# Kernel tuning notes

Hardware: AMD Instinct MI355X
Metric: run time of the kernel (lower is better)

## Reference

```python
import jax, jax.numpy as jnp
import numpy as np

T, B, LAG, H = 128, 1024, 6, 256


def setup_inputs() -> dict:
    key = jax.random.key(0)
    ks = jax.random.split(key, 16)
    s = 0.05  # small init scale to keep LSTM gates in a sane range
    d = {}
    d["x"] = jax.random.normal(ks[0], (T, B, LAG), jnp.float32)
    d["Wi1"] = jax.random.normal(ks[1], (H, LAG), jnp.float32) * s
    d["bi1"] = jnp.zeros((H,), jnp.float32)
    d["Wi2"] = jax.random.normal(ks[2], (H, H), jnp.float32) * s
    d["bi2"] = jnp.zeros((H,), jnp.float32)
    d["Wi3"] = jax.random.normal(ks[3], (H, H), jnp.float32) * s
    d["bi3"] = jnp.zeros((H,), jnp.float32)
    d["Wih0"] = jax.random.normal(ks[4], (4 * H, H), jnp.float32) * s
    d["Whh0"] = jax.random.normal(ks[5], (4 * H, H), jnp.float32) * s
    d["bih0"] = jnp.zeros((4 * H,), jnp.float32)
    d["bhh0"] = jnp.zeros((4 * H,), jnp.float32)
    d["Wih1"] = jax.random.normal(ks[6], (4 * H, H), jnp.float32) * s
    d["Whh1"] = jax.random.normal(ks[7], (4 * H, H), jnp.float32) * s
    d["bih1"] = jnp.zeros((4 * H,), jnp.float32)
    d["bhh1"] = jnp.zeros((4 * H,), jnp.float32)
    d["Wo1"] = jax.random.normal(ks[8], (H, H), jnp.float32) * s
    d["bo1"] = jnp.zeros((H,), jnp.float32)
    d["Wo2"] = jax.random.normal(ks[9], (H, H), jnp.float32) * s
    d["bo2"] = jnp.zeros((H,), jnp.float32)
    d["Wo3"] = jax.random.normal(ks[10], (LAG, H), jnp.float32) * s
    d["bo3"] = jnp.zeros((LAG,), jnp.float32)
    return d


def _lstm_cell(xt, h, c, Wih, Whh, bih, bhh):
    # PyTorch gate order: i, f, g, o
    g = xt @ Wih.T + h @ Whh.T + (bih + bhh)
    i, f, gg, o = jnp.split(g, 4, axis=-1)
    c2 = jax.nn.sigmoid(f) * c + jax.nn.sigmoid(i) * jnp.tanh(gg)
    h2 = jax.nn.sigmoid(o) * jnp.tanh(c2)
    return h2, c2


def reference(x, Wi1, bi1, Wi2, bi2, Wi3, bi3,
              Wih0, Whh0, bih0, bhh0, Wih1, Whh1, bih1, bhh1,
              Wo1, bo1, Wo2, bo2, Wo3, bo3):
    relu = jax.nn.relu
    # input MLP applied to every timestep at once: [T,B,6] -> [T,B,H]
    u = relu(x @ Wi1.T + bi1)
    u = relu(u @ Wi2.T + bi2)
    u = relu(u @ Wi3.T + bi3)

    def step(carry, xt):
        h0, c0, h1, c1 = carry
        h0, c0 = _lstm_cell(xt, h0, c0, Wih0, Whh0, bih0, bhh0)
        # dropout(0.05) between layers is identity in eval mode
        h1, c1 = _lstm_cell(h0, h1, c1, Wih1, Whh1, bih1, bhh1)
        return (h0, c0, h1, c1), h1

    z = jnp.zeros((x.shape[1], Whh0.shape[1]), x.dtype)
    _, hs = jax.lax.scan(step, (z, z, z, z), u)  # hs: [T,B,H]

    # output MLP: ReLU, Linear, ReLU, Linear, ReLU, Linear(H->6)
    y = relu(hs)
    y = relu(y @ Wo1.T + bo1)
    y = relu(y @ Wo2.T + bo2)
    y = y @ Wo3.T + bo3
    return y  # [T,B,6]
```

## Files before the change

kernel.cpp:

```cpp
#include <hip/hip_runtime.h>
#include <math.h>


namespace {
constexpr int kT   = 128;
constexpr int kB   = 1024;
constexpr int kLag = 6;
constexpr int kH   = 256;
constexpr int kTc  = 32;
constexpr int kMc  = kTc * kB;
constexpr int kGS  = 67;
constexpr int kLdsBytes = 2 * 32768 + 2 * 64 * kGS * 4;
}

typedef _Float16 half8 __attribute__((ext_vector_type(8)));
typedef _Float16 half2 __attribute__((ext_vector_type(2)));
typedef float f32x4 __attribute__((ext_vector_type(4)));
typedef unsigned long long u64;

__device__ __forceinline__ float sigm(float x) {
    return 1.f / (1.f + exp2f(-1.4426950408889634f * x));
}
__device__ __forceinline__ float tanh_(float x) {
    return 2.f / (1.f + exp2f(-2.8853900817779268f * x)) - 1.f;
}

__device__ __forceinline__ half8 pack(u64 a, u64 b) {
    union { u64 u[2]; half8 h; } r;
    r.u[0] = a; r.u[1] = b;
    return r.h;
}

__device__ __forceinline__ void ld_l2(half8& d, const _Float16* p) {
    asm volatile("global_load_dwordx4 %0, %1, off sc0"
                 : "=v"(d) : "v"(p) : "memory");
}
#define WAITCNT_HOLD8(A, B)                                                   \
    asm volatile("s_waitcnt vmcnt(0)"                                         \
        : "+v"(A[0]), "+v"(A[1]), "+v"(A[2]), "+v"(A[3]),                     \
          "+v"(B[0]), "+v"(B[1]), "+v"(B[2]), "+v"(B[3]))

__global__ __launch_bounds__(256)
void zero_fill(unsigned int* __restrict__ p)
{
    p[blockIdx.x * 256 + threadIdx.x] = 0u;
}

__global__ __launch_bounds__(256)
void cvt_f2h(const float* __restrict__ s, _Float16* __restrict__ d)
{
    const int i = blockIdx.x * 256 + threadIdx.x;
    d[i] = (_Float16)s[i];
}

__global__ __launch_bounds__(256)
void build_wcat(const float* __restrict__ Wih, const float* __restrict__ Whh,
                _Float16* __restrict__ d)
{
    const int i = blockIdx.x * 256 + threadIdx.x;
    const int row = i >> 9, col = i & 511;
    const float v = (col < 256) ? Wih[row * 256 + col] : Whh[row * 256 + col - 256];
    d[i] = (_Float16)v;
}

__global__ __launch_bounds__(256)
void add_bias(const float* __restrict__ a, const float* __restrict__ b,
              float* __restrict__ d)
{
    const int i = blockIdx.x * 256 + threadIdx.x;
    d[i] = a[i] + b[i];
}

__global__ __launch_bounds__(256)
void in_mlp1(const float* __restrict__ x, const float* __restrict__ Wi1,
             const float* __restrict__ bi1, _Float16* __restrict__ out)
{
    const int idx = blockIdx.x * 256 + threadIdx.x;
    const int col = idx & (kH - 1);
    const int row = idx >> 8;
    const float* xr = x + (size_t)row * kLag;
    const float* w  = Wi1 + col * kLag;
    float s = bi1[col];
#pragma unroll
    for (int k = 0; k < kLag; ++k) s = fmaf(xr[k], w[k], s);
    out[idx] = (_Float16)fmaxf(s, 0.f);
}

__global__ __launch_bounds__(256)
void gemm_h16(const _Float16* __restrict__ A, const _Float16* __restrict__ W,
              const float* __restrict__ bias, _Float16* __restrict__ C)
{
    const int tid = threadIdx.x;
    const int w = tid >> 6, lane = tid & 63, q = lane >> 4, l15 = lane & 15;
    const int n0 = blockIdx.x * 64;
    const int r0 = blockIdx.y * 128 + w * 32;

    half8 bf[4][8];
#pragma unroll
    for (int nt = 0; nt < 4; ++nt)
#pragma unroll
        for (int kk = 0; kk < 8; ++kk)
            bf[nt][kk] = *(const half8*)(W + (size_t)(n0 + nt * 16 + l15) * 256
                                         + kk * 32 + q * 8);
    float bz[4];
#pragma unroll
    for (int nt = 0; nt < 4; ++nt) bz[nt] = bias[n0 + nt * 16 + l15];

#pragma unroll
    for (int rt = 0; rt < 2; ++rt) {
        const _Float16* arow = A + (size_t)(r0 + rt * 16 + l15) * 256 + q * 8;
        half8 af[8];
#pragma unroll
        for (int kk = 0; kk < 8; ++kk) af[kk] = *(const half8*)(arow + kk * 32);
        f32x4 acc[4];
#pragma unroll
        for (int nt = 0; nt < 4; ++nt)
            acc[nt] = (f32x4){bz[nt], bz[nt], bz[nt], bz[nt]};
#pragma unroll
        for (int kk = 0; kk < 8; ++kk)
#pragma unroll
            for (int nt = 0; nt < 4; ++nt)
                acc[nt] = __builtin_amdgcn_mfma_f32_16x16x32_f16(
                    af[kk], bf[nt][kk], acc[nt], 0, 0, 0);
#pragma unroll
        for (int nt = 0; nt < 4; ++nt)
#pragma unroll
            for (int r = 0; r < 4; ++r) {
                const float v = fmaxf(acc[nt][r], 0.f);
                C[(size_t)(r0 + rt * 16 + q * 4 + r) * 256 + n0 + nt * 16 + l15]
                    = (_Float16)v;
            }
    }
}

__device__ __forceinline__ void xbar(unsigned int* __restrict__ cptr,
                                     unsigned int target, int tid)
{
    asm volatile("s_waitcnt vmcnt(0)" ::: "memory");
    __syncthreads();
    if (tid == 0) {
        __hip_atomic_fetch_add(cptr, 1u, __ATOMIC_RELAXED,
                               __HIP_MEMORY_SCOPE_AGENT);
        while (__hip_atomic_load(cptr, __ATOMIC_RELAXED,
                                 __HIP_MEMORY_SCOPE_AGENT) < target)
            __builtin_amdgcn_s_sleep(1);
    }
    __syncthreads();
}

__device__ __forceinline__ void gather_lo(const _Float16* lo, int row, int q,
                                          u64* ua)
{
    const u64* plo = (const u64*)(lo + (size_t)row * 256 + q * 8);
#pragma unroll
    for (int kk = 0; kk < 8; ++kk) {
        ua[2*kk]   = plo[kk*8];
        ua[2*kk+1] = plo[kk*8 + 1];
    }
}

__device__ __forceinline__ void gstore(float* __restrict__ gl, int m0, int nb,
                                       int q, int l15,
                                       const f32x4& a0, const f32x4& a1)
{
#pragma unroll
    for (int r = 0; r < 4; ++r) {
        gl[(m0 + q*4 + r) * kGS + nb + l15]      = a0[r];
        gl[(m0 + q*4 + r) * kGS + nb + 16 + l15] = a1[r];
    }
}

__device__ __forceinline__ void phase_gemm_lds2(
    const char* pA, const char* pB,
    const half8 (&B0)[16], const half8 (&B1)[16],
    float* __restrict__ gl, int rtb, int nb, int q, int l15)
{
#pragma unroll
    for (int rt = 0; rt < 2; ++rt) {
        const int row = (rtb + rt) * 16 + l15;
        const int xr  = ((row & 15) << 4) ^ ((row & 1) << 8);
        const int rb  = row * 512;
        f32x4 a0 = {0.f,0.f,0.f,0.f}, a1 = {0.f,0.f,0.f,0.f};
#pragma unroll
        for (int kk = 0; kk < 8; ++kk) {
            const int off = rb + ((q * 16 + kk * 64) ^ xr);
            const half8 alo = *(const half8*)(pA + off);
            const half8 ahi = *(const half8*)(pB + off);
            a0 = __builtin_amdgcn_mfma_f32_16x16x32_f16(alo, B0[kk],     a0, 0,0,0);
            a1 = __builtin_amdgcn_mfma_f32_16x16x32_f16(alo, B1[kk],     a1, 0,0,0);
            a0 = __builtin_amdgcn_mfma_f32_16x16x32_f16(ahi, B0[8 + kk], a0, 0,0,0);
            a1 = __builtin_amdgcn_mfma_f32_16x16x32_f16(ahi, B1[8 + kk], a1, 0,0,0);
        }
        gstore(gl, (rtb + rt) * 16, nb, q, l15, a0, a1);
    }
}

__device__ __forceinline__ void phase_gemm_l0(
    const _Float16* __restrict__ u, const char* pH0,
    const half8 (&B0)[16], const half8 (&B1)[16],
    float* __restrict__ gl, int rtb, int nb, int q, int l15)
{
#pragma unroll
    for (int rt = 0; rt < 2; ++rt) {
        const int row = (rtb + rt) * 16 + l15;
        const int xr  = ((row & 15) << 4) ^ ((row & 1) << 8);
        const int rb  = row * 512;
        const _Float16* pu = u + (size_t)row * 256 + q * 8;
        half8 uf[8];
#pragma unroll
        for (int kk = 0; kk < 8; ++kk) uf[kk] = *(const half8*)(pu + kk * 32);
        f32x4 a0 = {0.f,0.f,0.f,0.f}, a1 = {0.f,0.f,0.f,0.f};
#pragma unroll
        for (int kk = 0; kk < 8; ++kk) {
            const int off = rb + ((q * 16 + kk * 64) ^ xr);
            const half8 ah = *(const half8*)(pH0 + off);
            a0 = __builtin_amdgcn_mfma_f32_16x16x32_f16(uf[kk], B0[kk],   a0, 0,0,0);
            a1 = __builtin_amdgcn_mfma_f32_16x16x32_f16(uf[kk], B1[kk],   a1, 0,0,0);
            a0 = __builtin_amdgcn_mfma_f32_16x16x32_f16(ah, B0[8 + kk],   a0, 0,0,0);
            a1 = __builtin_amdgcn_mfma_f32_16x16x32_f16(ah, B1[8 + kk],   a1, 0,0,0);
        }
        gstore(gl, (rtb + rt) * 16, nb, q, l15, a0, a1);
    }
}

__device__ __forceinline__ void cell_one(const float* __restrict__ gl,
    int crow, int cc, const float* __restrict__ bs, float* __restrict__ cst,
    _Float16* __restrict__ hout, _Float16* __restrict__ uout)
{
    const float* gr = gl + crow * kGS;
    _Float16 hp[2];
#pragma unroll
    for (int e = 0; e < 2; ++e) {
        const float gi = gr[0*16 + cc + e] + bs[e*4 + 0];
        const float gf = gr[1*16 + cc + e] + bs[e*4 + 1];
        const float gg = gr[2*16 + cc + e] + bs[e*4 + 2];
        const float go = gr[3*16 + cc + e] + bs[e*4 + 3];
        const float c2 = sigm(gf) * cst[e] + sigm(gi) * tanh_(gg);
        cst[e] = c2;
        hp[e] = (_Float16)(sigm(go) * tanh_(c2));
    }
    *(half2*)(hout + (size_t)crow * 256 + cc) = (half2){hp[0], hp[1]};
    if (uout) {
        const _Float16 z = (_Float16)0.f;
        *(half2*)(uout + (size_t)crow * 256 + cc) =
            (half2){hp[0] > z ? hp[0] : z, hp[1] > z ? hp[1] : z};
    }
}

__global__ __launch_bounds__(512, 2)
void lstm_all(_Float16* __restrict__ ubuf,
              const _Float16* __restrict__ Wc0, const _Float16* __restrict__ Wc1,
              const float* __restrict__ bc0, const float* __restrict__ bc1,
              _Float16* __restrict__ h0b, _Float16* __restrict__ h1b,
              unsigned int* __restrict__ cnt)
{
    extern __shared__ char lds[];
    char* pH0  = lds;
    char* pH1  = lds + 32768;
    float* gl0 = (float*)(lds + 65536);
    float* gl1 = gl0 + 64 * kGS;

    const int tid = threadIdx.x;
    const int w = tid >> 6, lane = tid & 63, q = lane >> 4, l15 = lane & 15;
    const int wl = w & 3;
    const int rtb = (wl >> 1) * 2;
    const int nb  = (wl & 1) * 32;
    const int lyr = (w < 4) ? 1 : 0;

    __shared__ int sh_bi, sh_js;
    if (tid == 0) {
        unsigned int xcd = __builtin_amdgcn_s_getreg(20 | (31 << 11)) & 7u;
        unsigned int rank = __hip_atomic_fetch_add(cnt + 512 + xcd * 16, 1u,
            __ATOMIC_RELAXED, __HIP_MEMORY_SCOPE_AGENT);
        sh_bi = (int)(xcd * 2 + (rank >> 4));
        sh_js = (int)(rank & 15);
    }
    __syncthreads();
    const int bi = sh_bi, js = sh_js;
    unsigned int* cptr = cnt + bi * 32;

    const _Float16* WcL = lyr ? Wc1 : Wc0;
    half8 Bf0[16], Bf1[16];
    {
        const _Float16* wr0 = WcL
            + (size_t)((nb >> 4) * 256 + js * 16 + l15) * 512 + q * 8;
        const _Float16* wr1 = WcL
            + (size_t)(((nb >> 4) + 1) * 256 + js * 16 + l15) * 512 + q * 8;
#pragma unroll
        for (int kk = 0; kk < 16; ++kk) {
            Bf0[kk] = *(const half8*)(wr0 + kk * 32);
            Bf1[kk] = *(const half8*)(wr1 + kk * 32);
        }
    }

    int sdst[4];
#pragma unroll
    for (int r = 0; r < 4; ++r) {
        const int L   = tid * 16 + r * 8192;
        const int row = L >> 9;
        const int c   = L & 511;
        sdst[r] = row * 512 + (c ^ ((row & 15) << 4) ^ ((row & 1) << 8));
    }

    const int cc = (tid & 7) * 2;
    const int crow = tid >> 3;
    float bs0[8], bs1[8];
#pragma unroll
    for (int e = 0; e < 2; ++e)
#pragma unroll
        for (int g = 0; g < 4; ++g) {
            bs0[e*4 + g] = bc0[g * 256 + js * 16 + cc + e];
            bs1[e*4 + g] = bc1[g * 256 + js * 16 + cc + e];
        }
    float cst0[2] = {0.f, 0.f}, cst1[2] = {0.f, 0.f};
    const size_t rbase = (size_t)bi * 64 * 256;
    const size_t obase = rbase + js * 16;

    if (lyr == 0) {
#pragma unroll
        for (int rt = 0; rt < 2; ++rt) {
            u64 ua[16];
            gather_lo(ubuf + rbase, (rtb + rt) * 16 + l15, q, ua);
            f32x4 a0 = {0.f,0.f,0.f,0.f}, a1 = {0.f,0.f,0.f,0.f};
#pragma unroll
            for (int kk = 0; kk < 8; ++kk) {
                const half8 af = pack(ua[2*kk], ua[2*kk+1]);
                a0 = __builtin_amdgcn_mfma_f32_16x16x32_f16(af, Bf0[kk], a0, 0,0,0);
                a1 = __builtin_amdgcn_mfma_f32_16x16x32_f16(af, Bf1[kk], a1, 0,0,0);
            }
            gstore(gl0, (rtb + rt) * 16, nb, q, l15, a0, a1);
        }
    }
    __syncthreads();
    cell_one(gl0, crow, cc, bs0, cst0, h0b + obase, nullptr);
    xbar(cptr, 16u, tid);

    for (int t = 0; t < kT; ++t) {
        const size_t p  = (size_t)(t & 1) * kB * 256;
        const size_t pn = (size_t)((t & 1) ^ 1) * kB * 256;
        const bool hasB = (t < kT - 1);

        {
            half8 s0[4], s1h[4];
            const char* b0 = (const char*)(h0b + p  + rbase);
            const char* b1 = (const char*)(h1b + pn + rbase);
#pragma unroll
            for (int r = 0; r < 4; ++r) {
                ld_l2(s0[r],  (const _Float16*)(b0 + tid * 16 + r * 8192));
                ld_l2(s1h[r], (const _Float16*)(b1 + tid * 16 + r * 8192));
            }
            WAITCNT_HOLD8(s0, s1h);
#pragma unroll
            for (int r = 0; r < 4; ++r) {
                *(half8*)(pH0 + sdst[r]) = s0[r];
                *(half8*)(pH1 + sdst[r]) = s1h[r];
            }
        }
        __syncthreads();

        if (lyr == 1) {
            phase_gemm_lds2(pH0, pH1, Bf0, Bf1, gl1, rtb, nb, q, l15);
        } else if (hasB) {
            phase_gemm_l0(ubuf + (size_t)(t + 1) * kB * 256 + rbase, pH0,
                          Bf0, Bf1, gl0, rtb, nb, q, l15);
        }
        __syncthreads();

        cell_one(gl1, crow, cc, bs1, cst1, h1b + p + obase,
                 ubuf + (size_t)t * kB * 256 + obase);
        if (hasB) {
            cell_one(gl0, crow, cc, bs0, cst0, h0b + pn + obase, nullptr);
            xbar(cptr, (unsigned)(16 * (t + 2)), tid);
        }
    }
}

__global__ __launch_bounds__(256)
void out_mlp3(const _Float16* __restrict__ y2, const float* __restrict__ Wo3,
              const float* __restrict__ bo3, float* __restrict__ out)
{
    const int lane = threadIdx.x & 63;
    const int row  = blockIdx.x * 4 + (threadIdx.x >> 6);
    const _Float16* yr = y2 + (size_t)row * kH + lane * 4;
    const float a0 = (float)yr[0], a1 = (float)yr[1], a2 = (float)yr[2], a3 = (float)yr[3];
    float s[kLag];
#pragma unroll
    for (int o = 0; o < kLag; ++o) {
        const float4 wv = *(const float4*)(Wo3 + o * kH + lane * 4);
        s[o] = a0 * wv.x + a1 * wv.y + a2 * wv.z + a3 * wv.w;
    }
#pragma unroll
    for (int off = 32; off > 0; off >>= 1) {
#pragma unroll
        for (int o = 0; o < kLag; ++o) s[o] += __shfl_down(s[o], off);
    }
    if (lane == 0) {
#pragma unroll
        for (int o = 0; o < kLag; ++o)
            out[(size_t)row * kLag + o] = s[o] + bo3[o];
    }
}

extern "C" void kernel_launch(void* const* d_in, const int* in_sizes, int n_in,
                              void* d_out, int out_size, void* d_ws, size_t ws_size,
                              hipStream_t stream)
{
    const float* x    = (const float*)d_in[0];
    const float* Wi1  = (const float*)d_in[1];
    const float* bi1  = (const float*)d_in[2];
    const float* Wi2  = (const float*)d_in[3];
    const float* bi2  = (const float*)d_in[4];
    const float* Wi3  = (const float*)d_in[5];
    const float* bi3  = (const float*)d_in[6];
    const float* Wih0 = (const float*)d_in[7];
    const float* Whh0 = (const float*)d_in[8];
    const float* bih0 = (const float*)d_in[9];
    const float* bhh0 = (const float*)d_in[10];
    const float* Wih1 = (const float*)d_in[11];
    const float* Whh1 = (const float*)d_in[12];
    const float* bih1 = (const float*)d_in[13];
    const float* bhh1 = (const float*)d_in[14];
    const float* Wo1  = (const float*)d_in[15];
    const float* bo1  = (const float*)d_in[16];
    const float* Wo2  = (const float*)d_in[17];
    const float* bo2  = (const float*)d_in[18];
    const float* Wo3  = (const float*)d_in[19];
    const float* bo3  = (const float*)d_in[20];
    float* outp = (float*)d_out;

    char* p = (char*)d_ws;
    _Float16* ubuf = (_Float16*)p;  p += (size_t)kT * kB * kH * 2;
    _Float16* s1   = (_Float16*)p;  p += (size_t)kMc * kH * 2;
    _Float16* s2   = (_Float16*)p;  p += (size_t)kMc * kH * 2;
    _Float16* Wc0  = (_Float16*)p;  p += (size_t)1024 * 512 * 2;
    _Float16* Wc1  = (_Float16*)p;  p += (size_t)1024 * 512 * 2;
    _Float16* W2h  = (_Float16*)p;  p += (size_t)kH * kH * 2;
    _Float16* W3h  = (_Float16*)p;  p += (size_t)kH * kH * 2;
    _Float16* Wo1h = (_Float16*)p;  p += (size_t)kH * kH * 2;
    _Float16* Wo2h = (_Float16*)p;  p += (size_t)kH * kH * 2;
    float* bc0 = (float*)p;  p += 1024 * 4;
    float* bc1 = (float*)p;  p += 1024 * 4;
    _Float16* h0b = (_Float16*)p;  p += (size_t)2 * kB * kH * 2;
    _Float16* h1b = (_Float16*)p;  p += (size_t)2 * kB * kH * 2;
    unsigned int* cnt = (unsigned int*)p;  p += 4096;

    zero_fill<<<2052, 256, 0, stream>>>((unsigned int*)h0b);
    cvt_f2h<<<kH * kH / 256, 256, 0, stream>>>(Wi2, W2h);
    cvt_f2h<<<kH * kH / 256, 256, 0, stream>>>(Wi3, W3h);
    cvt_f2h<<<kH * kH / 256, 256, 0, stream>>>(Wo1, Wo1h);
    cvt_f2h<<<kH * kH / 256, 256, 0, stream>>>(Wo2, Wo2h);
    build_wcat<<<1024 * 512 / 256, 256, 0, stream>>>(Wih0, Whh0, Wc0);
    build_wcat<<<1024 * 512 / 256, 256, 0, stream>>>(Wih1, Whh1, Wc1);
    add_bias<<<4, 256, 0, stream>>>(bih0, bhh0, bc0);
    add_bias<<<4, 256, 0, stream>>>(bih1, bhh1, bc1);

    for (int c = 0; c < kT / kTc; ++c) {
        in_mlp1<<<kMc * kH / 256, 256, 0, stream>>>(
            x + (size_t)c * kMc * kLag, Wi1, bi1, s1);
        gemm_h16<<<dim3(4, kMc / 128), 256, 0, stream>>>(s1, W2h, bi2, s2);
        gemm_h16<<<dim3(4, kMc / 128), 256, 0, stream>>>(
            s2, W3h, bi3, ubuf + (size_t)c * kMc * kH);
    }

    static bool attr_set = false;
    if (!attr_set) {
        hipFuncSetAttribute((const void*)lstm_all,
                            hipFuncAttributeMaxDynamicSharedMemorySize, kLdsBytes);
        attr_set = true;
    }
    void* args[] = {&ubuf, &Wc0, &Wc1, &bc0, &bc1, &h0b, &h1b, &cnt};
    hipLaunchCooperativeKernel((const void*)lstm_all, dim3(256), dim3(512),
                               args, kLdsBytes, stream);

    for (int c = 0; c < kT / kTc; ++c) {
        gemm_h16<<<dim3(4, kMc / 128), 256, 0, stream>>>(
            ubuf + (size_t)c * kMc * kH, Wo1h, bo1, s1);
        gemm_h16<<<dim3(4, kMc / 128), 256, 0, stream>>>(s1, Wo2h, bo2, s2);
        out_mlp3<<<kMc / 4, 256, 0, stream>>>(
            s2, Wo3, bo3, outp + (size_t)c * kMc * kLag);
    }
}
```

Measured before the change: 1.993 ms.

## Replace shared-counter barrier with per-block flag slots and split arrive/wait

Replaces the single atomic counter barrier, where thread 0 increments and spins, with per-workgroup flag slots. Each block signals its own slot after finishing a step, and waits only at the start of the next step, polling all 16 peer slots in parallel with a wavefront vote. This is meant to cut atomic contention on one address and to move the wait point later so the tail of each step overlaps with peer skew. It also preloads all u fragments for both row tiles before the MFMA loop, and it enlarges and re-zeroes the counter workspace to hold the padded slots.

```diff
diff --git a/kernel.cpp b/kernel.cpp
--- a/kernel.cpp
+++ b/kernel.cpp
@@ -133,17 +133,16 @@
     }
 }
 
-__device__ __forceinline__ void xbar(unsigned int* __restrict__ cptr,
-                                     unsigned int target, int tid)
-{
-    asm volatile("s_waitcnt vmcnt(0)" ::: "memory");
-    __syncthreads();
-    if (tid == 0) {
-        __hip_atomic_fetch_add(cptr, 1u, __ATOMIC_RELAXED,
-                               __HIP_MEMORY_SCOPE_AGENT);
-        while (__hip_atomic_load(cptr, __ATOMIC_RELAXED,
-                                 __HIP_MEMORY_SCOPE_AGENT) < target)
-            __builtin_amdgcn_s_sleep(1);
+__device__ __forceinline__ void waitpeers(const unsigned int* __restrict__ fb,
+                                          unsigned int target, int tid)
+{
+    if (tid < 64) {
+        const unsigned int* fp = fb + (tid & 15) * 16;
+        unsigned int v;
+        do {
+            v = __hip_atomic_load(fp, __ATOMIC_RELAXED,
+                                  __HIP_MEMORY_SCOPE_AGENT);
+        } while (__any(v < target));
     }
     __syncthreads();
 }
@@ -200,24 +199,28 @@
     const half8 (&B0)[16], const half8 (&B1)[16],
     float* __restrict__ gl, int rtb, int nb, int q, int l15)
 {
+    half8 uf[2][8];
+#pragma unroll
+    for (int rt = 0; rt < 2; ++rt) {
+        const _Float16* pu = u + (size_t)((rtb + rt) * 16 + l15) * 256 + q * 8;
+#pragma unroll
+        for (int kk = 0; kk < 8; ++kk)
+            uf[rt][kk] = *(const half8*)(pu + kk * 32);
+    }
 #pragma unroll
     for (int rt = 0; rt < 2; ++rt) {
         const int row = (rtb + rt) * 16 + l15;
         const int xr  = ((row & 15) << 4) ^ ((row & 1) << 8);
         const int rb  = row * 512;
-        const _Float16* pu = u + (size_t)row * 256 + q * 8;
-        half8 uf[8];
-#pragma unroll
-        for (int kk = 0; kk < 8; ++kk) uf[kk] = *(const half8*)(pu + kk * 32);
         f32x4 a0 = {0.f,0.f,0.f,0.f}, a1 = {0.f,0.f,0.f,0.f};
 #pragma unroll
         for (int kk = 0; kk < 8; ++kk) {
             const int off = rb + ((q * 16 + kk * 64) ^ xr);
             const half8 ah = *(const half8*)(pH0 + off);
-            a0 = __builtin_amdgcn_mfma_f32_16x16x32_f16(uf[kk], B0[kk],   a0, 0,0,0);
-            a1 = __builtin_amdgcn_mfma_f32_16x16x32_f16(uf[kk], B1[kk],   a1, 0,0,0);
-            a0 = __builtin_amdgcn_mfma_f32_16x16x32_f16(ah, B0[8 + kk],   a0, 0,0,0);
-            a1 = __builtin_amdgcn_mfma_f32_16x16x32_f16(ah, B1[8 + kk],   a1, 0,0,0);
+            a0 = __builtin_amdgcn_mfma_f32_16x16x32_f16(uf[rt][kk], B0[kk], a0, 0,0,0);
+            a1 = __builtin_amdgcn_mfma_f32_16x16x32_f16(uf[rt][kk], B1[kk], a1, 0,0,0);
+            a0 = __builtin_amdgcn_mfma_f32_16x16x32_f16(ah, B0[8 + kk],     a0, 0,0,0);
+            a1 = __builtin_amdgcn_mfma_f32_16x16x32_f16(ah, B1[8 + kk],     a1, 0,0,0);
         }
         gstore(gl, (rtb + rt) * 16, nb, q, l15, a0, a1);
     }
@@ -270,14 +273,15 @@
     __shared__ int sh_bi, sh_js;
     if (tid == 0) {
         unsigned int xcd = __builtin_amdgcn_s_getreg(20 | (31 << 11)) & 7u;
-        unsigned int rank = __hip_atomic_fetch_add(cnt + 512 + xcd * 16, 1u,
+        unsigned int rank = __hip_atomic_fetch_add(cnt + 4096 + xcd * 16, 1u,
             __ATOMIC_RELAXED, __HIP_MEMORY_SCOPE_AGENT);
         sh_bi = (int)(xcd * 2 + (rank >> 4));
         sh_js = (int)(rank & 15);
     }
     __syncthreads();
     const int bi = sh_bi, js = sh_js;
-    unsigned int* cptr = cnt + bi * 32;
+    unsigned int* fb    = cnt + (size_t)bi * 256;
+    unsigned int* fslot = fb + js * 16;
 
     const _Float16* WcL = lyr ? Wc1 : Wc0;
     half8 Bf0[16], Bf1[16];
@@ -333,12 +337,18 @@
     }
     __syncthreads();
     cell_one(gl0, crow, cc, bs0, cst0, h0b + obase, nullptr);
-    xbar(cptr, 16u, tid);
+    asm volatile("s_waitcnt vmcnt(0)" ::: "memory");
+    __syncthreads();
+    if (tid == 0)
+        __hip_atomic_fetch_add(fslot, 1u, __ATOMIC_RELAXED,
+                               __HIP_MEMORY_SCOPE_AGENT);
 
     for (int t = 0; t < kT; ++t) {
         const size_t p  = (size_t)(t & 1) * kB * 256;
         const size_t pn = (size_t)((t & 1) ^ 1) * kB * 256;
         const bool hasB = (t < kT - 1);
+
+        waitpeers(fb, (unsigned)(t + 1), tid);
 
         {
             half8 s0[4], s1h[4];
@@ -370,7 +380,11 @@
                  ubuf + (size_t)t * kB * 256 + obase);
         if (hasB) {
             cell_one(gl0, crow, cc, bs0, cst0, h0b + pn + obase, nullptr);
-            xbar(cptr, (unsigned)(16 * (t + 2)), tid);
+            asm volatile("s_waitcnt vmcnt(0)" ::: "memory");
+            __syncthreads();
+            if (tid == 0)
+                __hip_atomic_fetch_add(fslot, 1u, __ATOMIC_RELAXED,
+                                       __HIP_MEMORY_SCOPE_AGENT);
         }
     }
 }
@@ -442,9 +456,9 @@
     float* bc1 = (float*)p;  p += 1024 * 4;
     _Float16* h0b = (_Float16*)p;  p += (size_t)2 * kB * kH * 2;
     _Float16* h1b = (_Float16*)p;  p += (size_t)2 * kB * kH * 2;
-    unsigned int* cnt = (unsigned int*)p;  p += 4096;
-
-    zero_fill<<<2052, 256, 0, stream>>>((unsigned int*)h0b);
+    unsigned int* cnt = (unsigned int*)p;  p += 17408;
+
+    zero_fill<<<2065, 256, 0, stream>>>((unsigned int*)h0b);
     cvt_f2h<<<kH * kH / 256, 256, 0, stream>>>(Wi2, W2h);
     cvt_f2h<<<kH * kH / 256, 256, 0, stream>>>(Wi3, W3h);
     cvt_f2h<<<kH * kH / 256, 256, 0, stream>>>(Wo1, Wo1h);
```

Measured after the change: 2.023 ms. No clear change (+1.5%).
